# Kernel optimization log

Measured on AMD Instinct MI355X. Metric: run time of the kernel, lower is better.

Reference implementation:

```python
import jax, jax.numpy as jnp
import numpy as np

MIN_C, MAX_C = 1e-4, 1e4
EPS_C = 1e-6
TAU = 1.0            # fixed temperature (learnable_temperature=False), clamp is a no-op here
NORM_EPS = 1e-15
ARTANH_EPS = 1e-7

B, C, D = 512, 512, 512


def _expmap0(u, sc):
    # geoopt expmap0 for k = -c: tanh(sqrt(c)*||u||) * u / (sqrt(c)*||u||)
    norm = jnp.maximum(jnp.linalg.norm(u, axis=-1, keepdims=True), NORM_EPS)
    return jnp.tanh(sc * norm) * u / (sc * norm)


def setup_inputs() -> dict:
    key = jax.random.key(0)
    k1, k2 = jax.random.split(key)
    euclidean_feats = jax.random.normal(k1, (B, D), dtype=jnp.float32) * 0.05
    proto_tan = jax.random.normal(k2, (C, D), dtype=jnp.float32) * 0.001  # proto_init_std
    raw_c = jnp.asarray(0.0, dtype=jnp.float32)  # log(init_curvature=1.0)
    return {"euclidean_feats": euclidean_feats, "proto_tan": proto_tan, "raw_c": raw_c}


def reference(euclidean_feats, proto_tan, raw_c):
    # current_c(): softplus(raw_c) + eps, clipped
    c = jnp.clip(jax.nn.softplus(raw_c) + EPS_C, MIN_C, MAX_C)
    sc = jnp.sqrt(c)

    z = _expmap0(euclidean_feats, sc)  # (B, D) points on Poincare ball
    p = _expmap0(proto_tan, sc)        # (C, D)

    # dist(z, p) = 2/sqrt(c) * artanh(sqrt(c) * || (-z) mobius_add p ||)
    x = -z                                      # (B, D)
    x2 = jnp.sum(x * x, axis=-1)[:, None]       # (B, 1)
    y2 = jnp.sum(p * p, axis=-1)[None, :]       # (1, C)
    xy = x @ p.T                                # (B, C) inner products (GEMM)

    # mobius_add with k = -c:
    # num = (1 + 2c<x,y> + c||y||^2) x + (1 - c||x||^2) y
    # den = 1 + 2c<x,y> + c^2 ||x||^2 ||y||^2
    num = ((1.0 + 2.0 * c * xy + c * y2)[..., None] * x[:, None, :]
           + (1.0 - c * x2)[..., None] * p[None, :, :])     # (B, C, D)
    den = jnp.maximum(1.0 + 2.0 * c * xy + (c * c) * x2 * y2, NORM_EPS)  # (B, C)
    m = num / den[..., None]

    mnorm = jnp.linalg.norm(m, axis=-1)  # (B, C)
    t = jnp.clip(sc * mnorm, -1.0 + ARTANH_EPS, 1.0 - ARTANH_EPS)
    d = (2.0 / sc) * jnp.arctanh(t)      # (B, C) hyperbolic distances

    return -d / TAU
```

## Files before the change

kernel.cpp:

```cpp
#include <hip/hip_runtime.h>
#include <math.h>

#define B_ 512
#define C_ 512
#define D_ 512

__device__ __forceinline__ float compute_c(const float* raw_c) {
    float rc = raw_c[0];
    float sp = fmaxf(rc, 0.0f) + log1pf(expf(-fabsf(rc)));
    float c = sp + 1e-6f;
    return fminf(fmaxf(c, 1e-4f), 1e4f);
}

__global__ __launch_bounds__(64) void prep_kernel(
    const float* __restrict__ feats, const float* __restrict__ protos,
    const float* __restrict__ raw_c,
    float* __restrict__ z, float* __restrict__ p,
    float* __restrict__ x2, float* __restrict__ y2)
{
    int row = blockIdx.x;
    const float* src;
    float* dst;
    float* sq;
    int r;
    if (row < B_) { r = row;      src = feats  + (size_t)r * D_; dst = z + (size_t)r * D_; sq = x2; }
    else          { r = row - B_; src = protos + (size_t)r * D_; dst = p + (size_t)r * D_; sq = y2; }

    float c = compute_c(raw_c);
    float scc = sqrtf(c);

    int lane = threadIdx.x;
    const float4* s4 = (const float4*)src;
    float4 v0 = s4[lane];
    float4 v1 = s4[lane + 64];
    float ss = v0.x*v0.x + v0.y*v0.y + v0.z*v0.z + v0.w*v0.w
             + v1.x*v1.x + v1.y*v1.y + v1.z*v1.z + v1.w*v1.w;
    #pragma unroll
    for (int off = 32; off > 0; off >>= 1) ss += __shfl_xor(ss, off);

    float n = fmaxf(sqrtf(ss), 1e-15f);
    float s = tanhf(scc * n) / (scc * n);

    float4* d4 = (float4*)dst;
    d4[lane]      = make_float4(v0.x*s, v0.y*s, v0.z*s, v0.w*s);
    d4[lane + 64] = make_float4(v1.x*s, v1.y*s, v1.z*s, v1.w*s);
    if (lane == 0) sq[r] = s * s * ss;
}

__device__ __forceinline__ float dist_val(float zp, float x2, float y2,
                                          float c, float scc, float inv_sc) {
    float xy = -zp;
    float two_cxy = 2.0f * c * xy;
    float a = 1.0f + two_cxy + c * y2;
    float b = 1.0f - c * x2;
    float den = fmaxf(1.0f + two_cxy + c * c * x2 * y2, 1e-15f);
    float num2 = a * a * x2 + 2.0f * a * b * xy + b * b * y2;
    float mn = sqrtf(fmaxf(num2, 0.0f)) / den;
    float t = fminf(scc * mn, 1.0f - 1e-7f);
    return -inv_sc * logf((1.0f + t) / (1.0f - t));
}

__global__ __launch_bounds__(256) void dist_kernel(
    const float* __restrict__ z, const float* __restrict__ p,
    const float* __restrict__ x2v, const float* __restrict__ y2v,
    const float* __restrict__ raw_c, float* __restrict__ out)
{
    __shared__ float As[32][33];
    __shared__ float Bs[32][33];

    int t  = threadIdx.x;
    int tx = t & 15;
    int ty = t >> 4;
    int row0 = blockIdx.y * 32;
    int col0 = blockIdx.x * 32;

    int lrow = t >> 3;
    int lc4  = (t & 7) * 4;

    float acc00 = 0.f, acc01 = 0.f, acc10 = 0.f, acc11 = 0.f;

    for (int k0 = 0; k0 < D_; k0 += 32) {
        float4 av = *(const float4*)(z + (size_t)(row0 + lrow) * D_ + k0 + lc4);
        float4 bv = *(const float4*)(p + (size_t)(col0 + lrow) * D_ + k0 + lc4);
        __syncthreads();
        As[lrow][lc4+0] = av.x; As[lrow][lc4+1] = av.y;
        As[lrow][lc4+2] = av.z; As[lrow][lc4+3] = av.w;
        Bs[lrow][lc4+0] = bv.x; Bs[lrow][lc4+1] = bv.y;
        Bs[lrow][lc4+2] = bv.z; Bs[lrow][lc4+3] = bv.w;
        __syncthreads();
        #pragma unroll
        for (int k = 0; k < 32; ++k) {
            float a0 = As[ty][k],      a1 = As[ty + 16][k];
            float b0 = Bs[tx][k],      b1 = Bs[tx + 16][k];
            acc00 = fmaf(a0, b0, acc00);
            acc01 = fmaf(a0, b1, acc01);
            acc10 = fmaf(a1, b0, acc10);
            acc11 = fmaf(a1, b1, acc11);
        }
    }

    float c = compute_c(raw_c);
    float scc = sqrtf(c);
    float inv_sc = 1.0f / scc;

    int i0 = row0 + ty, i1 = row0 + ty + 16;
    int j0 = col0 + tx, j1 = col0 + tx + 16;
    float x2_0 = x2v[i0], x2_1 = x2v[i1];
    float y2_0 = y2v[j0], y2_1 = y2v[j1];

    out[(size_t)i0 * C_ + j0] = dist_val(acc00, x2_0, y2_0, c, scc, inv_sc);
    out[(size_t)i0 * C_ + j1] = dist_val(acc01, x2_0, y2_1, c, scc, inv_sc);
    out[(size_t)i1 * C_ + j0] = dist_val(acc10, x2_1, y2_0, c, scc, inv_sc);
    out[(size_t)i1 * C_ + j1] = dist_val(acc11, x2_1, y2_1, c, scc, inv_sc);
}

extern "C" void kernel_launch(void* const* d_in, const int* in_sizes, int n_in,
                              void* d_out, int out_size, void* d_ws, size_t ws_size,
                              hipStream_t stream) {
    const float* feats  = (const float*)d_in[0];
    const float* protos = (const float*)d_in[1];
    const float* raw_c  = (const float*)d_in[2];
    float* out = (float*)d_out;

    float* z  = (float*)d_ws;
    float* p  = z + (size_t)B_ * D_;
    float* x2 = p + (size_t)C_ * D_;
    float* y2 = x2 + B_;

    prep_kernel<<<B_ + C_, 64, 0, stream>>>(feats, protos, raw_c, z, p, x2, y2);

    dim3 grid(C_ / 32, B_ / 32);
    dist_kernel<<<grid, 256, 0, stream>>>(z, p, x2, y2, raw_c, out);
}
```

Baseline: 79.09 us.

## Fuse expmap prep into distance kernel and use bf16 MFMA for inner products

Drops the separate prep kernel. Each 32x32 output tile now loads its raw feature and prototype rows, computes the expmap0 scaling and squared norms on chip, and stores the scaled rows as bf16 in shared memory. The inner products then come from bf16 MFMA 16x16x32 instructions instead of scalar FP32 FMAs. This removes one kernel launch and the workspace round trip, and moves the GEMM onto matrix cores. The cost is redundant prep work, since every tile recomputes norms for its rows. It also loses precision through bf16 rounding of the inner products, and a duplicated pair of conversion statements is left as dead code.

Result: faster. 66.62 us (-15.8%).

```diff
diff --git a/kernel.cpp b/kernel.cpp
--- a/kernel.cpp
+++ b/kernel.cpp
@@ -4,47 +4,22 @@
 #define B_ 512
 #define C_ 512
 #define D_ 512
+#define LDK 520
 
-__device__ __forceinline__ float compute_c(const float* raw_c) {
-    float rc = raw_c[0];
+typedef __attribute__((ext_vector_type(8))) short s8v;
+typedef __attribute__((ext_vector_type(4))) short s4v;
+typedef __attribute__((ext_vector_type(4))) float f4v;
+
+__device__ __forceinline__ float compute_c_dev(float rc) {
     float sp = fmaxf(rc, 0.0f) + log1pf(expf(-fabsf(rc)));
     float c = sp + 1e-6f;
     return fminf(fmaxf(c, 1e-4f), 1e4f);
 }
 
-__global__ __launch_bounds__(64) void prep_kernel(
-    const float* __restrict__ feats, const float* __restrict__ protos,
-    const float* __restrict__ raw_c,
-    float* __restrict__ z, float* __restrict__ p,
-    float* __restrict__ x2, float* __restrict__ y2)
-{
-    int row = blockIdx.x;
-    const float* src;
-    float* dst;
-    float* sq;
-    int r;
-    if (row < B_) { r = row;      src = feats  + (size_t)r * D_; dst = z + (size_t)r * D_; sq = x2; }
-    else          { r = row - B_; src = protos + (size_t)r * D_; dst = p + (size_t)r * D_; sq = y2; }
-
-    float c = compute_c(raw_c);
-    float scc = sqrtf(c);
-
-    int lane = threadIdx.x;
-    const float4* s4 = (const float4*)src;
-    float4 v0 = s4[lane];
-    float4 v1 = s4[lane + 64];
-    float ss = v0.x*v0.x + v0.y*v0.y + v0.z*v0.z + v0.w*v0.w
-             + v1.x*v1.x + v1.y*v1.y + v1.z*v1.z + v1.w*v1.w;
-    #pragma unroll
-    for (int off = 32; off > 0; off >>= 1) ss += __shfl_xor(ss, off);
-
-    float n = fmaxf(sqrtf(ss), 1e-15f);
-    float s = tanhf(scc * n) / (scc * n);
-
-    float4* d4 = (float4*)dst;
-    d4[lane]      = make_float4(v0.x*s, v0.y*s, v0.z*s, v0.w*s);
-    d4[lane + 64] = make_float4(v1.x*s, v1.y*s, v1.z*s, v1.w*s);
-    if (lane == 0) sq[r] = s * s * ss;
+__device__ __forceinline__ unsigned short f2bf(float f) {
+    unsigned u = __float_as_uint(f);
+    u += 0x7FFFu + ((u >> 16) & 1u);
+    return (unsigned short)(u >> 16);
 }
 
 __device__ __forceinline__ float dist_val(float zp, float x2, float y2,
@@ -60,58 +35,110 @@
     return -inv_sc * logf((1.0f + t) / (1.0f - t));
 }
 
-__global__ __launch_bounds__(256) void dist_kernel(
-    const float* __restrict__ z, const float* __restrict__ p,
-    const float* __restrict__ x2v, const float* __restrict__ y2v,
+__global__ __launch_bounds__(256, 1) void fused_kernel(
+    const float* __restrict__ feats, const float* __restrict__ protos,
     const float* __restrict__ raw_c, float* __restrict__ out)
 {
-    __shared__ float As[32][33];
-    __shared__ float Bs[32][33];
+    __shared__ short zs[32 * LDK];
+    __shared__ short ps[32 * LDK];
+    __shared__ float x2s[32];
+    __shared__ float y2s[32];
 
-    int t  = threadIdx.x;
-    int tx = t & 15;
-    int ty = t >> 4;
-    int row0 = blockIdx.y * 32;
-    int col0 = blockIdx.x * 32;
+    const int t    = threadIdx.x;
+    const int lane = t & 63;
+    const int w    = t >> 6;
+    const int row0 = blockIdx.y * 32;
+    const int col0 = blockIdx.x * 32;
 
-    int lrow = t >> 3;
-    int lc4  = (t & 7) * 4;
+    const float c      = compute_c_dev(raw_c[0]);
+    const float scc    = sqrtf(c);
+    const float inv_sc = 1.0f / scc;
 
-    float acc00 = 0.f, acc01 = 0.f, acc10 = 0.f, acc11 = 0.f;
-
-    for (int k0 = 0; k0 < D_; k0 += 32) {
-        float4 av = *(const float4*)(z + (size_t)(row0 + lrow) * D_ + k0 + lc4);
-        float4 bv = *(const float4*)(p + (size_t)(col0 + lrow) * D_ + k0 + lc4);
-        __syncthreads();
-        As[lrow][lc4+0] = av.x; As[lrow][lc4+1] = av.y;
-        As[lrow][lc4+2] = av.z; As[lrow][lc4+3] = av.w;
-        Bs[lrow][lc4+0] = bv.x; Bs[lrow][lc4+1] = bv.y;
-        Bs[lrow][lc4+2] = bv.z; Bs[lrow][lc4+3] = bv.w;
-        __syncthreads();
+    {
+        const float4* srcA = (const float4*)(feats + (size_t)(row0 + 8 * w) * D_);
+        float4 v0[8], v1[8];
         #pragma unroll
-        for (int k = 0; k < 32; ++k) {
-            float a0 = As[ty][k],      a1 = As[ty + 16][k];
-            float b0 = Bs[tx][k],      b1 = Bs[tx + 16][k];
-            acc00 = fmaf(a0, b0, acc00);
-            acc01 = fmaf(a0, b1, acc01);
-            acc10 = fmaf(a1, b0, acc10);
-            acc11 = fmaf(a1, b1, acc11);
+        for (int i = 0; i < 8; ++i) {
+            v0[i] = srcA[i * 128 + lane];
+            v1[i] = srcA[i * 128 + lane + 64];
+        }
+        #pragma unroll
+        for (int i = 0; i < 8; ++i) {
+            int r = 8 * w + i;
+            float ss = v0[i].x*v0[i].x + v0[i].y*v0[i].y + v0[i].z*v0[i].z + v0[i].w*v0[i].w
+                     + v1[i].x*v1[i].x + v1[i].y*v1[i].y + v1[i].z*v1[i].z + v1[i].w*v1[i].w;
+            #pragma unroll
+            for (int off = 32; off > 0; off >>= 1) ss += __shfl_xor(ss, off);
+            float n = fmaxf(sqrtf(ss), 1e-15f);
+            float s = tanhf(scc * n) / (scc * n);
+            if (lane == 0) x2s[r] = s * s * ss;
+            s4v lo, hi;
+            lo[0]=(short)f2bf(v0[i].x); lo[1]=(short)f2bf(v0[i].y);
+            lo[2]=(short)f2bf(v0[i].z); lo[3]=(short)f2bf(v0[i].w);
+            hi[0]=(short)f2bf(v1[i].x); hi[1]=(short)f2bf(v1[i].y);
+            hi[2]=(short)f2bf(v1[i].z); hi[3]=(short)f2bf(v1[i].w);
+            lo[0]=(short)f2bf(v0[i].x*s); lo[1]=(short)f2bf(v0[i].y*s);
+            lo[2]=(short)f2bf(v0[i].z*s); lo[3]=(short)f2bf(v0[i].w*s);
+            hi[0]=(short)f2bf(v1[i].x*s); hi[1]=(short)f2bf(v1[i].y*s);
+            hi[2]=(short)f2bf(v1[i].z*s); hi[3]=(short)f2bf(v1[i].w*s);
+            *(s4v*)(&zs[r * LDK + 4 * lane])       = lo;
+            *(s4v*)(&zs[r * LDK + 256 + 4 * lane]) = hi;
+        }
+    }
+    {
+        const float4* srcB = (const float4*)(protos + (size_t)(col0 + 8 * w) * D_);
+        float4 v0[8], v1[8];
+        #pragma unroll
+        for (int i = 0; i < 8; ++i) {
+            v0[i] = srcB[i * 128 + lane];
+            v1[i] = srcB[i * 128 + lane + 64];
+        }
+        #pragma unroll
+        for (int i = 0; i < 8; ++i) {
+            int r = 8 * w + i;
+            float ss = v0[i].x*v0[i].x + v0[i].y*v0[i].y + v0[i].z*v0[i].z + v0[i].w*v0[i].w
+                     + v1[i].x*v1[i].x + v1[i].y*v1[i].y + v1[i].z*v1[i].z + v1[i].w*v1[i].w;
+            #pragma unroll
+            for (int off = 32; off > 0; off >>= 1) ss += __shfl_xor(ss, off);
+            float n = fmaxf(sqrtf(ss), 1e-15f);
+            float s = tanhf(scc * n) / (scc * n);
+            if (lane == 0) y2s[r] = s * s * ss;
+            s4v lo, hi;
+            lo[0]=(short)f2bf(v0[i].x*s); lo[1]=(short)f2bf(v0[i].y*s);
+            lo[2]=(short)f2bf(v0[i].z*s); lo[3]=(short)f2bf(v0[i].w*s);
+            hi[0]=(short)f2bf(v1[i].x*s); hi[1]=(short)f2bf(v1[i].y*s);
+            hi[2]=(short)f2bf(v1[i].z*s); hi[3]=(short)f2bf(v1[i].w*s);
+            *(s4v*)(&ps[r * LDK + 4 * lane])       = lo;
+            *(s4v*)(&ps[r * LDK + 256 + 4 * lane]) = hi;
         }
     }
 
-    float c = compute_c(raw_c);
-    float scc = sqrtf(c);
-    float inv_sc = 1.0f / scc;
+    __syncthreads();
 
-    int i0 = row0 + ty, i1 = row0 + ty + 16;
-    int j0 = col0 + tx, j1 = col0 + tx + 16;
-    float x2_0 = x2v[i0], x2_1 = x2v[i1];
-    float y2_0 = y2v[j0], y2_1 = y2v[j1];
+    const int wr = w >> 1, wc = w & 1;
+    const int rowA = 16 * wr + (lane & 15);
+    const int rowB = 16 * wc + (lane & 15);
+    const short* za = &zs[rowA * LDK + 8 * (lane >> 4)];
+    const short* pa = &ps[rowB * LDK + 8 * (lane >> 4)];
 
-    out[(size_t)i0 * C_ + j0] = dist_val(acc00, x2_0, y2_0, c, scc, inv_sc);
-    out[(size_t)i0 * C_ + j1] = dist_val(acc01, x2_0, y2_1, c, scc, inv_sc);
-    out[(size_t)i1 * C_ + j0] = dist_val(acc10, x2_1, y2_0, c, scc, inv_sc);
-    out[(size_t)i1 * C_ + j1] = dist_val(acc11, x2_1, y2_1, c, scc, inv_sc);
+    f4v acc = {0.f, 0.f, 0.f, 0.f};
+    #pragma unroll
+    for (int kk = 0; kk < 16; ++kk) {
+        s8v af = *(const s8v*)(za + kk * 32);
+        s8v bf = *(const s8v*)(pa + kk * 32);
+        acc = __builtin_amdgcn_mfma_f32_16x16x32_bf16(af, bf, acc, 0, 0, 0);
+    }
+
+    const int col   = lane & 15;
+    const int rbase = 4 * (lane >> 4);
+    const int gcol  = col0 + 16 * wc + col;
+    const float y2  = y2s[16 * wc + col];
+    #pragma unroll
+    for (int r = 0; r < 4; ++r) {
+        int lrow = 16 * wr + rbase + r;
+        float x2 = x2s[lrow];
+        out[(size_t)(row0 + lrow) * C_ + gcol] = dist_val(acc[r], x2, y2, c, scc, inv_sc);
+    }
 }
 
 extern "C" void kernel_launch(void* const* d_in, const int* in_sizes, int n_in,
@@ -122,13 +149,6 @@
     const float* raw_c  = (const float*)d_in[2];
     float* out = (float*)d_out;
 
-    float* z  = (float*)d_ws;
-    float* p  = z + (size_t)B_ * D_;
-    float* x2 = p + (size_t)C_ * D_;
-    float* y2 = x2 + B_;
-
-    prep_kernel<<<B_ + C_, 64, 0, stream>>>(feats, protos, raw_c, z, p, x2, y2);
-
     dim3 grid(C_ / 32, B_ / 32);
-    dist_kernel<<<grid, 256, 0, stream>>>(z, p, x2, y2, raw_c, out);
+    fused_kernel<<<grid, 256, 0, stream>>>(feats, protos, raw_c, out);
 }
```
